# Kernel optimization log

Measured on AMD Instinct MI355X. Metric: run time of the kernel, lower is better.

## Reference

```python
import jax, jax.numpy as jnp
import numpy as np

N = 20000      # nodes
E = 320000     # edges
F = 128        # feat_dim
N_RBF = 20
CUTOFF = 5.0


def setup_inputs() -> dict:
    key = jax.random.key(0)
    ks = jax.random.split(key, 12)
    h_i = jax.random.normal(ks[0], (N, F), dtype=jnp.float32)
    v_i = jax.random.normal(ks[1], (N, F, 3), dtype=jnp.float32)
    # distances in (0, cutoff); keep strictly > 0 to avoid div-by-zero in sinc basis
    d_ij = (jax.random.uniform(ks[2], (E,), dtype=jnp.float32) * 0.98 + 0.01) * CUTOFF
    r = jax.random.normal(ks[3], (E, 3), dtype=jnp.float32)
    unit_r_ij = r / jnp.linalg.norm(r, axis=-1, keepdims=True)
    nbrs = jax.random.randint(ks[4], (E, 2), 0, N, dtype=jnp.int64)
    # params: layers = Dense(F->F, swish) then Dense(F->3F); dist_embed dense: n_rbf -> 3F
    s1 = 1.0 / np.sqrt(F)
    W1 = jax.random.uniform(ks[5], (F, F), jnp.float32, -s1, s1)
    b1 = jax.random.uniform(ks[6], (F,), jnp.float32, -s1, s1)
    W2 = jax.random.uniform(ks[7], (F, 3 * F), jnp.float32, -s1, s1)
    b2 = jax.random.uniform(ks[8], (3 * F,), jnp.float32, -s1, s1)
    sr = 1.0 / np.sqrt(N_RBF)
    Wr = jax.random.uniform(ks[9], (N_RBF, 3 * F), jnp.float32, -sr, sr)
    br = jax.random.uniform(ks[10], (3 * F,), jnp.float32, -sr, sr)
    return {"h_i": h_i, "v_i": v_i, "d_ij": d_ij, "unit_r_ij": unit_r_ij,
            "nbrs": nbrs, "W1": W1, "b1": b1, "W2": W2, "b2": b2, "Wr": Wr, "br": br}


def _dist_embed(d, Wr, br):
    # PaiNN sinc-like radial basis: sin(n*pi*d/cutoff)/d, n=1..N_RBF
    n = jnp.arange(1, N_RBF + 1, dtype=d.dtype)
    rbf = jnp.sin(n[None, :] * jnp.pi * d[:, None] / CUTOFF) / d[:, None]  # [E, N_RBF]
    # cosine cutoff envelope
    fcut = 0.5 * (jnp.cos(jnp.pi * d / CUTOFF) + 1.0) * (d < CUTOFF)       # [E]
    return (rbf @ Wr + br) * fcut[:, None]                                  # [E, 3F]


def reference(h_i, v_i, d_ij, unit_r_ij, nbrs, W1, b1, W2, b2, Wr, br):
    # phi = Dense(swish) -> Dense : [N, 3F]
    phi = jax.nn.silu(h_i @ W1 + b1) @ W2 + b2
    src = nbrs[:, 1]
    dst = nbrs[:, 0]
    edge_inv = phi[src] * _dist_embed(d_ij, Wr, br)          # [E, 3F]
    edge_inv = edge_inv.reshape(edge_inv.shape[0], 3, F)     # [E, 3, F]
    f1, f2, f3 = edge_inv[:, 0], edge_inv[:, 1], edge_inv[:, 2]
    # dv: [E, F, 3]
    dv = f1[:, :, None] * unit_r_ij[:, None, :] + f2[:, :, None] * v_i[src]
    dh_i = jax.ops.segment_sum(f3, dst, num_segments=N)      # [N, F]
    dv_i = jax.ops.segment_sum(dv, dst, num_segments=N)      # [N, F, 3]
    return (dh_i, dv_i)
```

## Files before the change

kernel.cpp:

```cpp
#include <hip/hip_runtime.h>
#include <math.h>

#define F 128
#define THREEF 384
#define N_RBF 20
#define CUTOFF 5.0f
#define CAP 64
#define TLDS_STRIDE 136

typedef __bf16 bf16x8 __attribute__((ext_vector_type(8)));
typedef float  f32x4  __attribute__((ext_vector_type(4)));

__global__ __launch_bounds__(256) void prep_kernel(
    const float* __restrict__ d_ij, const float* __restrict__ unit_r,
    const int* __restrict__ nbrs,
    const float* __restrict__ W1, const float* __restrict__ W2,
    const float* __restrict__ Wr,
    int* __restrict__ cnt, float* __restrict__ pack,
    __bf16* __restrict__ W1T, __bf16* __restrict__ W2T,
    float* __restrict__ WrT, int E, int EB)
{
    const int tid = threadIdx.x;
    const int b   = blockIdx.x;

    if (b < EB) {
        const int e = b * 256 + tid;
        if (e >= E) return;
        const int2 nb = ((const int2*)nbrs)[e];
        const int dst = nb.x;
        const int src = nb.y;
        const int slot = atomicAdd(&cnt[dst], 1);
        if (slot >= CAP) return;

        const float d = d_ij[e];
        const float x = (float)M_PI * d * (1.0f / CUTOFF);
        float sx, cx;
        __sincosf(x, &sx, &cx);
        const float fcut = (d < CUTOFF) ? 0.5f * (cx + 1.0f) : 0.0f;
        float4 q0, q1;
        q0.x = sx * fcut / d;
        q0.y = 2.0f * cx;
        q0.z = fcut;
        q0.w = unit_r[3 * e + 0];
        q1.x = unit_r[3 * e + 1];
        q1.y = unit_r[3 * e + 2];
        q1.z = __int_as_float(src);
        q1.w = 0.0f;
        float4* pk = (float4*)(pack + ((size_t)dst * CAP + slot) * 8);
        pk[0] = q0;
        pk[1] = q1;
    } else if (b < EB + 256) {
        const int idx = (b - EB) * 256 + tid;
        if (idx < 128 * 128) {
            const int n = idx >> 7, k = idx & 127;
            W1T[idx] = (__bf16)W1[k * F + n];
        }
        if (idx < 384 * 128) {
            const int n = idx >> 7, k = idx & 127;
            W2T[idx] = (__bf16)W2[k * THREEF + n];
        }
    } else {
        const int idx = (b - EB - 256) * 256 + tid;
        if (idx >= 5 * 3 * 128) return;
        const int f  = idx & 127;
        const int c  = (idx >> 7) % 3;
        const int n4 = idx / (3 * 128);
        float4 v;
        v.x = Wr[(4 * n4 + 0) * THREEF + c * 128 + f];
        v.y = Wr[(4 * n4 + 1) * THREEF + c * 128 + f];
        v.z = Wr[(4 * n4 + 2) * THREEF + c * 128 + f];
        v.w = Wr[(4 * n4 + 3) * THREEF + c * 128 + f];
        ((float4*)WrT)[idx] = v;
    }
}

__global__ __launch_bounds__(256) void mlp_mfma_kernel(
    const float* __restrict__ h,
    const __bf16* __restrict__ W1T,
    const float* __restrict__ b1,
    const __bf16* __restrict__ W2T,
    const float* __restrict__ b2,
    float* __restrict__ phi, int N)
{
    __shared__ __bf16 t_lds[16 * TLDS_STRIDE];

    const int wave = threadIdx.x >> 6;
    const int lane = threadIdx.x & 63;
    const int m    = lane & 15;
    const int quad = lane >> 4;
    const int node0 = blockIdx.x * 16;
    if (node0 >= N) return;

    bf16x8 a1[4];
    #pragma unroll
    for (int kb = 0; kb < 4; ++kb) {
        const float* hp = h + (size_t)(node0 + m) * F + kb * 32 + quad * 8;
        const float4 x0 = *(const float4*)hp;
        const float4 x1 = *(const float4*)(hp + 4);
        bf16x8 a;
        a[0] = (__bf16)x0.x; a[1] = (__bf16)x0.y;
        a[2] = (__bf16)x0.z; a[3] = (__bf16)x0.w;
        a[4] = (__bf16)x1.x; a[5] = (__bf16)x1.y;
        a[6] = (__bf16)x1.z; a[7] = (__bf16)x1.w;
        a1[kb] = a;
    }

    #pragma unroll
    for (int c2 = 0; c2 < 2; ++c2) {
        const int ct = wave * 2 + c2;
        f32x4 acc = {0.0f, 0.0f, 0.0f, 0.0f};
        #pragma unroll
        for (int kb = 0; kb < 4; ++kb) {
            const bf16x8 b =
                *(const bf16x8*)(W1T + (size_t)(ct * 16 + m) * F + kb * 32 + quad * 8);
            acc = __builtin_amdgcn_mfma_f32_16x16x32_bf16(a1[kb], b, acc, 0, 0, 0);
        }
        const int col = ct * 16 + m;
        const float bb = b1[col];
        #pragma unroll
        for (int reg = 0; reg < 4; ++reg) {
            const float x = acc[reg] + bb;
            const float s = x / (1.0f + __expf(-x));
            t_lds[(quad * 4 + reg) * TLDS_STRIDE + col] = (__bf16)s;
        }
    }
    __syncthreads();

    bf16x8 a2[4];
    #pragma unroll
    for (int kb = 0; kb < 4; ++kb)
        a2[kb] = *(const bf16x8*)&t_lds[m * TLDS_STRIDE + kb * 32 + quad * 8];

    #pragma unroll
    for (int c6 = 0; c6 < 6; ++c6) {
        const int ct = c6 * 4 + wave;
        f32x4 acc = {0.0f, 0.0f, 0.0f, 0.0f};
        #pragma unroll
        for (int kb = 0; kb < 4; ++kb) {
            const bf16x8 b =
                *(const bf16x8*)(W2T + (size_t)(ct * 16 + m) * F + kb * 32 + quad * 8);
            acc = __builtin_amdgcn_mfma_f32_16x16x32_bf16(a2[kb], b, acc, 0, 0, 0);
        }
        const int col   = ct * 16 + m;
        const int plane = col >> 7;
        const int fc    = col & 127;
        const float bb  = b2[col];
        float* pp = phi + (size_t)plane * N * F + fc;
        #pragma unroll
        for (int reg = 0; reg < 4; ++reg) {
            const int row = quad * 4 + reg;
            pp[(size_t)(node0 + row) * F] = acc[reg] + bb;
        }
    }
}

__global__ __launch_bounds__(256) void gather_kernel(
    const float* __restrict__ phi,
    const float* __restrict__ v_i,
    const float* __restrict__ WrT,
    const float* __restrict__ br,
    const int*   __restrict__ cnt,
    const float* __restrict__ pack,
    float* __restrict__ dh,
    float* __restrict__ dv,
    int N)
{
    __shared__ float4 s_pack[2][CAP * 2];

    const int tid  = threadIdx.x;
    const int half = tid >> 7;
    const int f    = tid & 127;
    const int node = blockIdx.x * 2 + half;

    const int deg0 = cnt[node];
    const int deg  = deg0 < CAP ? deg0 : CAP;

    {
        const float4* src = (const float4*)(pack + (size_t)node * CAP * 8);
        if (f < 2 * deg) s_pack[half][f] = src[f];
    }
    __syncthreads();

    const float br0 = br[f], br1 = br[f + 128], br2 = br[f + 256];

    const float* phi0 = phi;
    const float* phi1 = phi + (size_t)N * F;
    const float* phi2 = phi + (size_t)2 * N * F;
    const float4* wT  = (const float4*)WrT;

    float dh_acc = 0.0f, dv0 = 0.0f, dv1 = 0.0f, dv2 = 0.0f;

    for (int i = 0; i < deg; ++i) {
        const float* q = (const float*)&s_pack[half][2 * i];
        const float s1   = q[0];
        const float twoc = q[1];
        const float fcut = q[2];
        const float ux   = q[3];
        const float uy   = q[4];
        const float uz   = q[5];
        const int src = __builtin_amdgcn_readfirstlane(__float_as_int(q[6]));

        float a0 = br0 * fcut, a1 = br1 * fcut, a2 = br2 * fcut;
        float rp = 0.0f, rc = s1;
        #pragma unroll
        for (int n4 = 0; n4 < 5; ++n4) {
            const float4 w0 = wT[(n4 * 3 + 0) * 128 + f];
            const float4 w1 = wT[(n4 * 3 + 1) * 128 + f];
            const float4 w2 = wT[(n4 * 3 + 2) * 128 + f];
            #pragma unroll
            for (int k = 0; k < 4; ++k) {
                const float wa = ((const float*)&w0)[k];
                const float wb = ((const float*)&w1)[k];
                const float wc = ((const float*)&w2)[k];
                a0 = fmaf(rc, wa, a0);
                a1 = fmaf(rc, wb, a1);
                a2 = fmaf(rc, wc, a2);
                const float rn = fmaf(twoc, rc, -rp);
                rp = rc;
                rc = rn;
            }
        }

        const float f1 = phi0[(size_t)src * F + f] * a0;
        const float f2 = phi1[(size_t)src * F + f] * a1;
        const float f3 = phi2[(size_t)src * F + f] * a2;

        dh_acc += f3;

        const float* vs = v_i + (size_t)src * THREEF + 3 * f;
        dv0 = fmaf(f1, ux, fmaf(f2, vs[0], dv0));
        dv1 = fmaf(f1, uy, fmaf(f2, vs[1], dv1));
        dv2 = fmaf(f1, uz, fmaf(f2, vs[2], dv2));
    }

    dh[(size_t)node * F + f] = dh_acc;
    float* dvp = dv + (size_t)node * THREEF + 3 * f;
    dvp[0] = dv0;
    dvp[1] = dv1;
    dvp[2] = dv2;
}

extern "C" void kernel_launch(void* const* d_in, const int* in_sizes, int n_in,
                              void* d_out, int out_size, void* d_ws, size_t ws_size,
                              hipStream_t stream) {
    const float* h_i    = (const float*)d_in[0];
    const float* v_i    = (const float*)d_in[1];
    const float* d_ij   = (const float*)d_in[2];
    const float* unit_r = (const float*)d_in[3];
    const int*   nbrs   = (const int*)  d_in[4];
    const float* W1     = (const float*)d_in[5];
    const float* b1     = (const float*)d_in[6];
    const float* W2     = (const float*)d_in[7];
    const float* b2     = (const float*)d_in[8];
    const float* Wr     = (const float*)d_in[9];
    const float* br     = (const float*)d_in[10];

    const int N = in_sizes[0] / F;
    const int E = in_sizes[2];

    float* dh = (float*)d_out;
    float* dv = dh + (size_t)N * F;

    float*  phi  = (float*)d_ws;
    float*  pack = phi + (size_t)3 * N * F;
    float*  WrT  = pack + (size_t)N * CAP * 8;
    int*    cnt  = (int*)(WrT + 5 * 3 * 128 * 4);
    __bf16* W1T  = (__bf16*)(cnt + N);
    __bf16* W2T  = W1T + 128 * 128;

    const int EB = (E + 255) / 256;

    hipMemsetAsync(cnt, 0, (size_t)N * sizeof(int), stream);

    prep_kernel<<<EB + 256 + 8, 256, 0, stream>>>(
        d_ij, unit_r, nbrs, W1, W2, Wr, cnt, pack, W1T, W2T, WrT, E, EB);
    mlp_mfma_kernel<<<(N + 15) / 16, 256, 0, stream>>>(h_i, W1T, b1, W2T, b2,
                                                       phi, N);
    gather_kernel<<<N / 2, 256, 0, stream>>>(phi, v_i, WrT, br, cnt, pack,
                                             dh, dv, N);
}
```

Measured before the change: 290.3 us.

## Merge edge packing with MLP kernel and precompute RBF basis in LDS

Weight transposes and the zeroing of the count array now run together in one init kernel, which replaces the memset. Edge packing and the MFMA MLP then share a single launch with disjoint block ranges, so the two can run concurrently. In the gather kernel, each edge's 20 Chebyshev-recurrence RBF values are computed once per node-half and stored in LDS, instead of being recomputed serially by all 128 feature threads. This trades a serial FMA dependency chain for LDS float4 reads, at the cost of an extra barrier and about 10KB more shared memory, which may lower occupancy.

```diff
diff --git a/kernel.cpp b/kernel.cpp
--- a/kernel.cpp
+++ b/kernel.cpp
@@ -11,15 +11,57 @@
 typedef __bf16 bf16x8 __attribute__((ext_vector_type(8)));
 typedef float  f32x4  __attribute__((ext_vector_type(4)));
 
-__global__ __launch_bounds__(256) void prep_kernel(
+__global__ __launch_bounds__(256) void init_kernel(
+    const float* __restrict__ W1, const float* __restrict__ W2,
+    const float* __restrict__ Wr,
+    __bf16* __restrict__ W1T, __bf16* __restrict__ W2T,
+    float* __restrict__ WrT, int* __restrict__ cnt, int N)
+{
+    const int tid = threadIdx.x;
+    const int b   = blockIdx.x;
+
+    if (b < 256) {
+        const int idx = b * 256 + tid;
+        if (idx < 128 * 128) {
+            const int n = idx >> 7, k = idx & 127;
+            W1T[idx] = (__bf16)W1[k * F + n];
+        }
+        if (idx < 384 * 128) {
+            const int n = idx >> 7, k = idx & 127;
+            W2T[idx] = (__bf16)W2[k * THREEF + n];
+        }
+    } else if (b < 264) {
+        const int idx = (b - 256) * 256 + tid;
+        if (idx >= 5 * 3 * 128) return;
+        const int f  = idx & 127;
+        const int c  = (idx >> 7) % 3;
+        const int n4 = idx / (3 * 128);
+        float4 v;
+        v.x = Wr[(4 * n4 + 0) * THREEF + c * 128 + f];
+        v.y = Wr[(4 * n4 + 1) * THREEF + c * 128 + f];
+        v.z = Wr[(4 * n4 + 2) * THREEF + c * 128 + f];
+        v.w = Wr[(4 * n4 + 3) * THREEF + c * 128 + f];
+        ((float4*)WrT)[idx] = v;
+    } else {
+        const int i = (b - 264) * 256 + tid;
+        if (i < (N + 3) / 4) {
+            int4 z; z.x = 0; z.y = 0; z.z = 0; z.w = 0;
+            ((int4*)cnt)[i] = z;
+        }
+    }
+}
+
+__global__ __launch_bounds__(256) void work_kernel(
     const float* __restrict__ d_ij, const float* __restrict__ unit_r,
     const int* __restrict__ nbrs,
-    const float* __restrict__ W1, const float* __restrict__ W2,
-    const float* __restrict__ Wr,
     int* __restrict__ cnt, float* __restrict__ pack,
-    __bf16* __restrict__ W1T, __bf16* __restrict__ W2T,
-    float* __restrict__ WrT, int E, int EB)
+    const float* __restrict__ h,
+    const __bf16* __restrict__ W1T, const float* __restrict__ b1,
+    const __bf16* __restrict__ W2T, const float* __restrict__ b2,
+    float* __restrict__ phi, int E, int EB, int N)
 {
+    __shared__ __bf16 t_lds[16 * TLDS_STRIDE];
+
     const int tid = threadIdx.x;
     const int b   = blockIdx.x;
 
@@ -49,46 +91,14 @@
         float4* pk = (float4*)(pack + ((size_t)dst * CAP + slot) * 8);
         pk[0] = q0;
         pk[1] = q1;
-    } else if (b < EB + 256) {
-        const int idx = (b - EB) * 256 + tid;
-        if (idx < 128 * 128) {
-            const int n = idx >> 7, k = idx & 127;
-            W1T[idx] = (__bf16)W1[k * F + n];
-        }
-        if (idx < 384 * 128) {
-            const int n = idx >> 7, k = idx & 127;
-            W2T[idx] = (__bf16)W2[k * THREEF + n];
-        }
-    } else {
-        const int idx = (b - EB - 256) * 256 + tid;
-        if (idx >= 5 * 3 * 128) return;
-        const int f  = idx & 127;
-        const int c  = (idx >> 7) % 3;
-        const int n4 = idx / (3 * 128);
-        float4 v;
-        v.x = Wr[(4 * n4 + 0) * THREEF + c * 128 + f];
-        v.y = Wr[(4 * n4 + 1) * THREEF + c * 128 + f];
-        v.z = Wr[(4 * n4 + 2) * THREEF + c * 128 + f];
-        v.w = Wr[(4 * n4 + 3) * THREEF + c * 128 + f];
-        ((float4*)WrT)[idx] = v;
-    }
-}
-
-__global__ __launch_bounds__(256) void mlp_mfma_kernel(
-    const float* __restrict__ h,
-    const __bf16* __restrict__ W1T,
-    const float* __restrict__ b1,
-    const __bf16* __restrict__ W2T,
-    const float* __restrict__ b2,
-    float* __restrict__ phi, int N)
-{
-    __shared__ __bf16 t_lds[16 * TLDS_STRIDE];
-
-    const int wave = threadIdx.x >> 6;
-    const int lane = threadIdx.x & 63;
+        return;
+    }
+
+    const int wave = tid >> 6;
+    const int lane = tid & 63;
     const int m    = lane & 15;
     const int quad = lane >> 4;
-    const int node0 = blockIdx.x * 16;
+    const int node0 = (b - EB) * 16;
     if (node0 >= N) return;
 
     bf16x8 a1[4];
@@ -111,9 +121,9 @@
         f32x4 acc = {0.0f, 0.0f, 0.0f, 0.0f};
         #pragma unroll
         for (int kb = 0; kb < 4; ++kb) {
-            const bf16x8 b =
+            const bf16x8 bb =
                 *(const bf16x8*)(W1T + (size_t)(ct * 16 + m) * F + kb * 32 + quad * 8);
-            acc = __builtin_amdgcn_mfma_f32_16x16x32_bf16(a1[kb], b, acc, 0, 0, 0);
+            acc = __builtin_amdgcn_mfma_f32_16x16x32_bf16(a1[kb], bb, acc, 0, 0, 0);
         }
         const int col = ct * 16 + m;
         const float bb = b1[col];
@@ -137,9 +147,9 @@
         f32x4 acc = {0.0f, 0.0f, 0.0f, 0.0f};
         #pragma unroll
         for (int kb = 0; kb < 4; ++kb) {
-            const bf16x8 b =
+            const bf16x8 bb =
                 *(const bf16x8*)(W2T + (size_t)(ct * 16 + m) * F + kb * 32 + quad * 8);
-            acc = __builtin_amdgcn_mfma_f32_16x16x32_bf16(a2[kb], b, acc, 0, 0, 0);
+            acc = __builtin_amdgcn_mfma_f32_16x16x32_bf16(a2[kb], bb, acc, 0, 0, 0);
         }
         const int col   = ct * 16 + m;
         const int plane = col >> 7;
@@ -166,6 +176,7 @@
     int N)
 {
     __shared__ float4 s_pack[2][CAP * 2];
+    __shared__ float  s_rbf[2][CAP * 20];
 
     const int tid  = threadIdx.x;
     const int half = tid >> 7;
@@ -181,6 +192,21 @@
     }
     __syncthreads();
 
+    if (f < deg) {
+        const float* q = (const float*)&s_pack[half][2 * f];
+        float rp = 0.0f, rc = q[0];
+        const float twoc = q[1];
+        float* rb = &s_rbf[half][f * 20];
+        rb[0] = rc;
+        #pragma unroll
+        for (int n = 1; n < 20; ++n) {
+            const float rn = fmaf(twoc, rc, -rp);
+            rp = rc; rc = rn;
+            rb[n] = rn;
+        }
+    }
+    __syncthreads();
+
     const float br0 = br[f], br1 = br[f + 128], br2 = br[f + 256];
 
     const float* phi0 = phi;
@@ -191,34 +217,33 @@
     float dh_acc = 0.0f, dv0 = 0.0f, dv1 = 0.0f, dv2 = 0.0f;
 
     for (int i = 0; i < deg; ++i) {
-        const float* q = (const float*)&s_pack[half][2 * i];
-        const float s1   = q[0];
-        const float twoc = q[1];
-        const float fcut = q[2];
-        const float ux   = q[3];
-        const float uy   = q[4];
-        const float uz   = q[5];
-        const int src = __builtin_amdgcn_readfirstlane(__float_as_int(q[6]));
+        const float4 q0 = s_pack[half][2 * i];
+        const float4 q1 = s_pack[half][2 * i + 1];
+        const float fcut = q0.z;
+        const float ux   = q0.w;
+        const float uy   = q1.x;
+        const float uz   = q1.y;
+        const int src = __builtin_amdgcn_readfirstlane(__float_as_int(q1.z));
 
         float a0 = br0 * fcut, a1 = br1 * fcut, a2 = br2 * fcut;
-        float rp = 0.0f, rc = s1;
         #pragma unroll
         for (int n4 = 0; n4 < 5; ++n4) {
             const float4 w0 = wT[(n4 * 3 + 0) * 128 + f];
             const float4 w1 = wT[(n4 * 3 + 1) * 128 + f];
             const float4 w2 = wT[(n4 * 3 + 2) * 128 + f];
-            #pragma unroll
-            for (int k = 0; k < 4; ++k) {
-                const float wa = ((const float*)&w0)[k];
-                const float wb = ((const float*)&w1)[k];
-                const float wc = ((const float*)&w2)[k];
-                a0 = fmaf(rc, wa, a0);
-                a1 = fmaf(rc, wb, a1);
-                a2 = fmaf(rc, wc, a2);
-                const float rn = fmaf(twoc, rc, -rp);
-                rp = rc;
-                rc = rn;
-            }
+            const float4 rb = *(const float4*)&s_rbf[half][i * 20 + n4 * 4];
+            a0 = fmaf(rb.x, w0.x, a0);
+            a1 = fmaf(rb.x, w1.x, a1);
+            a2 = fmaf(rb.x, w2.x, a2);
+            a0 = fmaf(rb.y, w0.y, a0);
+            a1 = fmaf(rb.y, w1.y, a1);
+            a2 = fmaf(rb.y, w2.y, a2);
+            a0 = fmaf(rb.z, w0.z, a0);
+            a1 = fmaf(rb.z, w1.z, a1);
+            a2 = fmaf(rb.z, w2.z, a2);
+            a0 = fmaf(rb.w, w0.w, a0);
+            a1 = fmaf(rb.w, w1.w, a1);
+            a2 = fmaf(rb.w, w2.w, a2);
         }
 
         const float f1 = phi0[(size_t)src * F + f] * a0;
@@ -269,13 +294,14 @@
     __bf16* W2T  = W1T + 128 * 128;
 
     const int EB = (E + 255) / 256;
-
-    hipMemsetAsync(cnt, 0, (size_t)N * sizeof(int), stream);
-
-    prep_kernel<<<EB + 256 + 8, 256, 0, stream>>>(
-        d_ij, unit_r, nbrs, W1, W2, Wr, cnt, pack, W1T, W2T, WrT, E, EB);
-    mlp_mfma_kernel<<<(N + 15) / 16, 256, 0, stream>>>(h_i, W1T, b1, W2T, b2,
-                                                       phi, N);
+    const int MB = (N + 15) / 16;
+    const int ZB = ((N + 3) / 4 + 255) / 256;
+
+    init_kernel<<<256 + 8 + ZB, 256, 0, stream>>>(W1, W2, Wr, W1T, W2T, WrT,
+                                                  cnt, N);
+    work_kernel<<<EB + MB, 256, 0, stream>>>(d_ij, unit_r, nbrs, cnt, pack,
+                                             h_i, W1T, b1, W2T, b2, phi,
+                                             E, EB, N);
     gather_kernel<<<N / 2, 256, 0, stream>>>(phi, v_i, WrT, br, cnt, pack,
                                              dh, dv, N);
 }
```

Result: no change. 293.8 us (+1.2%).
